# Performance work log

Hardware: AMD Instinct MI355X
Metric: run time of the kernel (lower is better)

Reference implementation:

```python
import jax, jax.numpy as jnp
import numpy as np

N_ITERS = 10
LR = 0.5
EPS = 1e-7


def _project(x):
    # project onto unit sphere: x / ||x||
    return x / jnp.maximum(jnp.linalg.norm(x, axis=-1, keepdims=True), EPS)


def _log_map(p, q):
    # p: (B, D) base points, q: (B, N, D) targets -> tangent vectors (B, N, D)
    cos = jnp.clip(jnp.einsum('bd,bnd->bn', p, q), -1.0 + EPS, 1.0 - EPS)
    theta = jnp.arccos(cos)                      # (B, N)
    u = q - cos[..., None] * p[:, None, :]       # component orthogonal to p
    unorm = jnp.maximum(jnp.linalg.norm(u, axis=-1), EPS)
    return (theta / unorm)[..., None] * u


def _exp_map(p, v):
    # p: (B, D), v: (B, D) tangent -> point on sphere (B, D)
    t = jnp.linalg.norm(v, axis=-1, keepdims=True)
    ts = jnp.maximum(t, EPS)
    return jnp.cos(t) * p + (jnp.sin(t) / ts) * v


def setup_inputs() -> dict:
    key = jax.random.key(0)
    k1, k2 = jax.random.split(key)
    B, N, D = 256, 1024, 256
    points = jax.random.normal(k1, (B, N, D), dtype=jnp.float32)
    points = points / jnp.linalg.norm(points, axis=-1, keepdims=True)  # on sphere
    weights = jax.random.uniform(k2, (B, N), dtype=jnp.float32) + 0.1
    return {"points": points, "weights": weights}


def reference(points, weights):
    # weighted Frechet mean on the sphere via Riemannian gradient descent
    w = weights / jnp.sum(weights, axis=-1, keepdims=True)  # (B, N)
    mean = _project(jnp.einsum('bn,bnd->bd', w, points))    # Euclidean init, projected
    for _ in range(N_ITERS):
        logs = _log_map(mean, points)                       # (B, N, D)
        grad = jnp.einsum('bn,bnd->bd', w, logs)            # weighted tangent mean
        mean = _exp_map(mean, LR * grad)
    return mean
```

## Files before the change

kernel.cpp:

```cpp
#include <hip/hip_runtime.h>
#include <math.h>

#define BB 256
#define NN 1024
#define DD 256
#define NWAVES 16
#define THREADS (NWAVES * 64)
#define PPW (NN / NWAVES)
#define CACHE_WAVES 2
#define CACHEP (CACHE_WAVES * PPW)
#define N_ITERS_C 10
#define LR_C 0.5f
#define EPS_C 1e-7f

__device__ __forceinline__ float wsum64(float v) {
    #pragma unroll
    for (int off = 32; off; off >>= 1) v += __shfl_xor(v, off, 64);
    return v;
}

__global__ __launch_bounds__(THREADS, 1)
void frechet_mean_kernel(const float* __restrict__ points,
                         const float* __restrict__ weights,
                         float* __restrict__ out) {
    const int b = blockIdx.x;
    const int w = threadIdx.x >> 6;
    const int lane = threadIdx.x & 63;
    const int lane4 = lane * 4;

    __shared__ float cacheQ[CACHEP][DD];
    __shared__ float waveAcc[NWAVES][DD];
    __shared__ float wLds[NN];
    __shared__ float waveS[NWAVES];

    const float* __restrict__ Qb = points + (size_t)b * NN * DD;
    const float* __restrict__ Wb = weights + (size_t)b * NN;
    const float* rowBase = Qb + (size_t)(w * PPW) * DD + lane4;

    wLds[threadIdx.x] = Wb[threadIdx.x];
    __syncthreads();

    float ax = 0.f, ay = 0.f, az = 0.f, aww = 0.f, swt = 0.f;
    #pragma unroll 4
    for (int i = 0; i < PPW; ++i) {
        const float4 q = *(const float4*)(rowBase + (size_t)i * DD);
        if (w < CACHE_WAVES)
            *(float4*)(&cacheQ[w * PPW + i][lane4]) = q;
        const float wt = wLds[w * PPW + i];
        ax = fmaf(wt, q.x, ax);
        ay = fmaf(wt, q.y, ay);
        az = fmaf(wt, q.z, az);
        aww = fmaf(wt, q.w, aww);
        swt += wt;
    }
    *(float4*)(&waveAcc[w][lane4]) = make_float4(ax, ay, az, aww);
    if (lane == 0) waveS[w] = swt;
    __syncthreads();

    float gx = 0.f, gy = 0.f, gz = 0.f, gw = 0.f, wsumTot = 0.f;
    #pragma unroll
    for (int j = 0; j < NWAVES; ++j) {
        const float4 t = *(const float4*)(&waveAcc[j][lane4]);
        gx += t.x; gy += t.y; gz += t.z; gw += t.w;
        wsumTot += waveS[j];
    }
    const float wsumInv = 1.0f / wsumTot;
    gx *= wsumInv; gy *= wsumInv; gz *= wsumInv; gw *= wsumInv;

    const float nrm2 = wsum64(gx * gx + gy * gy + gz * gz + gw * gw);
    const float rn = 1.0f / fmaxf(sqrtf(nrm2), EPS_C);
    float px = gx * rn, py = gy * rn, pz = gz * rn, pw = gw * rn;
    float pp = wsum64(px * px + py * py + pz * pz + pw * pw);

    const float CLIP = 1.0f - 1e-7f;

    for (int it = 0; it < N_ITERS_C; ++it) {
        __syncthreads();
        float accx = 0.f, accy = 0.f, accz = 0.f, accw = 0.f, s = 0.f;

        auto process2 = [&](const float4 q0, const float wc0,
                            const float4 q1, const float wc1) {
            float d0 = fmaf(q0.x, px, fmaf(q0.y, py, fmaf(q0.z, pz, q0.w * pw)));
            float d1 = fmaf(q1.x, px, fmaf(q1.y, py, fmaf(q1.z, pz, q1.w * pw)));
            #pragma unroll
            for (int off = 32; off; off >>= 1) {
                d0 += __shfl_xor(d0, off, 64);
                d1 += __shfl_xor(d1, off, 64);
            }
            const float c0v = fminf(fmaxf(d0, -CLIP), CLIP);
            const float c1v = fminf(fmaxf(d1, -CLIP), CLIP);
            const float th0 = acosf(c0v);
            const float th1 = acosf(c1v);
            float u0 = fmaf(c0v * c0v, pp, fmaf(-2.0f * c0v, d0, 1.0f));
            float u1 = fmaf(c1v * c1v, pp, fmaf(-2.0f * c1v, d1, 1.0f));
            const float c0 = wc0 * th0 * rsqrtf(fmaxf(u0, 1e-14f));
            const float c1 = wc1 * th1 * rsqrtf(fmaxf(u1, 1e-14f));
            accx = fmaf(c0, q0.x, fmaf(c1, q1.x, accx));
            accy = fmaf(c0, q0.y, fmaf(c1, q1.y, accy));
            accz = fmaf(c0, q0.z, fmaf(c1, q1.z, accz));
            accw = fmaf(c0, q0.w, fmaf(c1, q1.w, accw));
            s = fmaf(c0, c0v, fmaf(c1, c1v, s));
        };

        if (w < CACHE_WAVES) {
            #pragma unroll 2
            for (int i = 0; i < PPW; i += 2) {
                const float4 q0 = *(const float4*)(&cacheQ[w * PPW + i][lane4]);
                const float4 q1 = *(const float4*)(&cacheQ[w * PPW + i + 1][lane4]);
                process2(q0, wLds[w * PPW + i], q1, wLds[w * PPW + i + 1]);
            }
        } else {
            #pragma unroll 2
            for (int i = 0; i < PPW; i += 2) {
                const float4 q0 = *(const float4*)(rowBase + (size_t)i * DD);
                const float4 q1 = *(const float4*)(rowBase + (size_t)(i + 1) * DD);
                process2(q0, wLds[w * PPW + i], q1, wLds[w * PPW + i + 1]);
            }
        }

        *(float4*)(&waveAcc[w][lane4]) = make_float4(accx, accy, accz, accw);
        if (lane == 0) waveS[w] = s;
        __syncthreads();

        float grx = 0.f, gry = 0.f, grz = 0.f, grw = 0.f, sTot = 0.f;
        #pragma unroll
        for (int j = 0; j < NWAVES; ++j) {
            const float4 t = *(const float4*)(&waveAcc[j][lane4]);
            grx += t.x; gry += t.y; grz += t.z; grw += t.w;
            sTot += waveS[j];
        }
        const float scale = LR_C * wsumInv;
        const float vx = scale * (grx - sTot * px);
        const float vy = scale * (gry - sTot * py);
        const float vz = scale * (grz - sTot * pz);
        const float vw = scale * (grw - sTot * pw);

        const float t2 = wsum64(vx * vx + vy * vy + vz * vz + vw * vw);
        const float tn = sqrtf(t2);
        const float ts = fmaxf(tn, EPS_C);
        const float ct = cosf(tn);
        const float st = sinf(tn) / ts;
        px = ct * px + st * vx;
        py = ct * py + st * vy;
        pz = ct * pz + st * vz;
        pw = ct * pw + st * vw;
        pp = wsum64(px * px + py * py + pz * pz + pw * pw);
    }

    if (w == 0)
        *(float4*)(out + (size_t)b * DD + lane4) =
            make_float4(px, py, pz, pw);
}

extern "C" void kernel_launch(void* const* d_in, const int* in_sizes, int n_in,
                              void* d_out, int out_size, void* d_ws, size_t ws_size,
                              hipStream_t stream) {
    const float* points = (const float*)d_in[0];
    const float* weights = (const float*)d_in[1];
    float* out = (float*)d_out;
    (void)in_sizes; (void)n_in; (void)out_size; (void)d_ws; (void)ws_size;
    hipLaunchKernelGGL(frechet_mean_kernel, dim3(BB), dim3(THREADS), 0, stream,
                       points, weights, out);
}
```

Before: 702.6 us.

## Spread LDS cache across all waves, software-pipeline global loads, cheap acos polynomial

Instead of two waves caching all their points in LDS while the other fourteen stream from memory, every wave now caches its first 8 points. That balances load-imbalance across waves. The streaming loop is software-pipelined with loads issued two pairs ahead to hide global latency. acosf is replaced by an odd polynomial for |c|<=0.5, with a fallback to acosf otherwise. This risks small accuracy differences and some register pressure.

Result: faster. 671.0 us (-4.5%).

```diff
diff --git a/kernel.cpp b/kernel.cpp
--- a/kernel.cpp
+++ b/kernel.cpp
@@ -5,10 +5,10 @@
 #define NN 1024
 #define DD 256
 #define NWAVES 16
-#define THREADS (NWAVES * 64)
-#define PPW (NN / NWAVES)
-#define CACHE_WAVES 2
-#define CACHEP (CACHE_WAVES * PPW)
+#define THREADS 1024
+#define PPW 64
+#define CPW 8
+#define CACHEP (NWAVES * CPW)
 #define N_ITERS_C 10
 #define LR_C 0.5f
 #define EPS_C 1e-7f
@@ -17,6 +17,17 @@
     #pragma unroll
     for (int off = 32; off; off >>= 1) v += __shfl_xor(v, off, 64);
     return v;
+}
+
+__device__ __forceinline__ float theta_from_cos(float c) {
+    if (__builtin_expect(fabsf(c) > 0.5f, 0)) return acosf(c);
+    const float c2 = c * c;
+    float p = fmaf(c2, 0.022372159f, 0.030381944f);
+    p = fmaf(c2, p, 0.044642857f);
+    p = fmaf(c2, p, 0.075f);
+    p = fmaf(c2, p, 0.16666667f);
+    p = fmaf(c2, p, 1.0f);
+    return fmaf(-c, p, 1.57079632679f);
 }
 
 __global__ __launch_bounds__(THREADS, 1)
@@ -41,16 +52,21 @@
     __syncthreads();
 
     float ax = 0.f, ay = 0.f, az = 0.f, aww = 0.f, swt = 0.f;
+    #pragma unroll
+    for (int j = 0; j < CPW; ++j) {
+        const float4 q = *(const float4*)(rowBase + (size_t)j * DD);
+        *(float4*)(&cacheQ[w * CPW + j][lane4]) = q;
+        const float wt = wLds[w * PPW + j];
+        ax = fmaf(wt, q.x, ax); ay = fmaf(wt, q.y, ay);
+        az = fmaf(wt, q.z, az); aww = fmaf(wt, q.w, aww);
+        swt += wt;
+    }
     #pragma unroll 4
-    for (int i = 0; i < PPW; ++i) {
-        const float4 q = *(const float4*)(rowBase + (size_t)i * DD);
-        if (w < CACHE_WAVES)
-            *(float4*)(&cacheQ[w * PPW + i][lane4]) = q;
-        const float wt = wLds[w * PPW + i];
-        ax = fmaf(wt, q.x, ax);
-        ay = fmaf(wt, q.y, ay);
-        az = fmaf(wt, q.z, az);
-        aww = fmaf(wt, q.w, aww);
+    for (int j = CPW; j < PPW; ++j) {
+        const float4 q = *(const float4*)(rowBase + (size_t)j * DD);
+        const float wt = wLds[w * PPW + j];
+        ax = fmaf(wt, q.x, ax); ay = fmaf(wt, q.y, ay);
+        az = fmaf(wt, q.z, az); aww = fmaf(wt, q.w, aww);
         swt += wt;
     }
     *(float4*)(&waveAcc[w][lane4]) = make_float4(ax, ay, az, aww);
@@ -89,8 +105,8 @@
             }
             const float c0v = fminf(fmaxf(d0, -CLIP), CLIP);
             const float c1v = fminf(fmaxf(d1, -CLIP), CLIP);
-            const float th0 = acosf(c0v);
-            const float th1 = acosf(c1v);
+            const float th0 = theta_from_cos(c0v);
+            const float th1 = theta_from_cos(c1v);
             float u0 = fmaf(c0v * c0v, pp, fmaf(-2.0f * c0v, d0, 1.0f));
             float u1 = fmaf(c1v * c1v, pp, fmaf(-2.0f * c1v, d1, 1.0f));
             const float c0 = wc0 * th0 * rsqrtf(fmaxf(u0, 1e-14f));
@@ -102,21 +118,27 @@
             s = fmaf(c0, c0v, fmaf(c1, c1v, s));
         };
 
-        if (w < CACHE_WAVES) {
-            #pragma unroll 2
-            for (int i = 0; i < PPW; i += 2) {
-                const float4 q0 = *(const float4*)(&cacheQ[w * PPW + i][lane4]);
-                const float4 q1 = *(const float4*)(&cacheQ[w * PPW + i + 1][lane4]);
-                process2(q0, wLds[w * PPW + i], q1, wLds[w * PPW + i + 1]);
-            }
-        } else {
-            #pragma unroll 2
-            for (int i = 0; i < PPW; i += 2) {
-                const float4 q0 = *(const float4*)(rowBase + (size_t)i * DD);
-                const float4 q1 = *(const float4*)(rowBase + (size_t)(i + 1) * DD);
-                process2(q0, wLds[w * PPW + i], q1, wLds[w * PPW + i + 1]);
-            }
+        float4 a0 = *(const float4*)(rowBase + (size_t)8 * DD);
+        float4 a1 = *(const float4*)(rowBase + (size_t)9 * DD);
+        float4 b0 = *(const float4*)(rowBase + (size_t)10 * DD);
+        float4 b1 = *(const float4*)(rowBase + (size_t)11 * DD);
+
+        #pragma unroll
+        for (int j = 0; j < CPW; j += 2) {
+            const float4 q0 = *(const float4*)(&cacheQ[w * CPW + j][lane4]);
+            const float4 q1 = *(const float4*)(&cacheQ[w * CPW + j + 1][lane4]);
+            process2(q0, wLds[w * PPW + j], q1, wLds[w * PPW + j + 1]);
         }
+
+        #pragma unroll 2
+        for (int j = CPW; j < PPW - 4; j += 2) {
+            const float4 n0 = *(const float4*)(rowBase + (size_t)(j + 4) * DD);
+            const float4 n1 = *(const float4*)(rowBase + (size_t)(j + 5) * DD);
+            process2(a0, wLds[w * PPW + j], a1, wLds[w * PPW + j + 1]);
+            a0 = b0; a1 = b1; b0 = n0; b1 = n1;
+        }
+        process2(a0, wLds[w * PPW + PPW - 4], a1, wLds[w * PPW + PPW - 3]);
+        process2(b0, wLds[w * PPW + PPW - 2], b1, wLds[w * PPW + PPW - 1]);
 
         *(float4*)(&waveAcc[w][lane4]) = make_float4(accx, accy, accz, accw);
         if (lane == 0) waveS[w] = s;
```
